# Performance work log

Hardware: AMD Instinct MI355X
Metric: run time of the kernel (lower is better)

## Reference

```python
import jax, jax.numpy as jnp
import numpy as np

B, T, C, H = 4, 4096, 1024, 64

def setup_inputs() -> dict:
    key = jax.random.key(0)
    k1, k2, k3, k4 = jax.random.split(key, 4)
    x = jax.random.normal(k1, (B, T, C), dtype=jnp.float32)
    # Linear(n_embed, head_size, bias=False), stored as [in, out] for x @ W
    s = 1.0 / np.sqrt(C)
    Wq = jax.random.uniform(k2, (C, H), dtype=jnp.float32, minval=-s, maxval=s)
    Wk = jax.random.uniform(k3, (C, H), dtype=jnp.float32, minval=-s, maxval=s)
    Wv = jax.random.uniform(k4, (C, H), dtype=jnp.float32, minval=-s, maxval=s)
    return {"x": x, "Wq": Wq, "Wk": Wk, "Wv": Wv}

def reference(x, Wq, Wk, Wv):
    Bn, Tn, Cn = x.shape
    q = x @ Wq  # [B,T,H]
    k = x @ Wk  # [B,T,H]
    v = x @ Wv  # [B,T,H]
    # NOTE: original scales by C**-0.5 (embedding dim), not head_size**-0.5
    wei = jnp.einsum('bqh,bkh->bqk', q, k) * (Cn ** -0.5)  # [B,T,T]
    causal = jnp.tril(jnp.ones((Tn, Tn), dtype=bool))
    wei = jnp.where(causal, wei, -jnp.inf)
    wei = jax.nn.softmax(wei, axis=-1)
    out = jnp.einsum('bqk,bkh->bqh', wei, v)  # [B,T,H]
    return out
```

## Files before the change

### kernel.cpp

```cpp
#include <hip/hip_runtime.h>
#include <hip/hip_bf16.h>


#define B_DIM 4
#define T_DIM 4096
#define C_DIM 1024
#define H_DIM 64
#define SCALE2 0.0450842066f
#define KP 72

typedef __attribute__((ext_vector_type(8))) short bf8;
typedef __attribute__((ext_vector_type(4))) float f32x4;
typedef __attribute__((ext_vector_type(16))) float f32x16;

__device__ __forceinline__ float fast_exp2(float f) {
    return __builtin_amdgcn_exp2f(f);
}
__device__ __forceinline__ ushort f2bf(float f) {
    union { float f; uint u; } x; x.f = f;
    const uint u = x.u;
    return (ushort)((u + 0x7FFFu + ((u >> 16) & 1u)) >> 16);
}
__device__ __forceinline__ uint cvt_pk_bf16(float lo, float hi) {
    uint r;
    asm("v_cvt_pk_bf16_f32 %0, %1, %2" : "=v"(r) : "v"(lo), "v"(hi));
    return r;
}
__device__ __forceinline__ void permswapf(float& a, float& b) {
    asm volatile("v_permlane32_swap_b32 %0, %1" : "+v"(a), "+v"(b));
}
__device__ __forceinline__ void permswapu(uint& a, uint& b) {
    asm volatile("v_permlane32_swap_b32 %0, %1" : "+v"(a), "+v"(b));
}
__device__ __forceinline__ bf8 frag_from(uint w0, uint w1, uint w2, uint w3) {
    union { uint u[4]; bf8 f; } x;
    x.u[0] = w0; x.u[1] = w1; x.u[2] = w2; x.u[3] = w3;
    return x.f;
}

__global__ __launch_bounds__(256) void wt_kernel(
    const float* __restrict__ Wq, const float* __restrict__ Wk,
    const float* __restrict__ Wv, ushort* __restrict__ wtg)
{
    const int id  = blockIdx.x * 256 + threadIdx.x;
    const int col = id >> 7;
    const int k8  = (id & 127) * 8;
    const int m   = col >> 6, lc = col & 63;
    const float* W = (m == 0) ? Wq : (m == 1) ? Wk : Wv;
    ushort o[8];
    #pragma unroll
    for (int i = 0; i < 8; ++i)
        o[i] = f2bf(W[(size_t)(k8 + i) * H_DIM + lc]);
    *(bf8*)&wtg[(size_t)col * C_DIM + k8] = *(bf8*)o;
}

__global__ __launch_bounds__(256) void qkv_mfma_kernel(
    const float* __restrict__ x, const ushort* __restrict__ wtg,
    ushort* __restrict__ qo, ushort* __restrict__ ko, ushort* __restrict__ vo)
{
    __shared__ ushort xs[32][KP];
    __shared__ ushort wts[192][KP];
    const int t    = threadIdx.x;
    const int lane = t & 63, wave = t >> 6;
    const int g    = lane >> 4, lid = lane & 15;
    const size_t r0 = (size_t)blockIdx.x * 32;

    f32x4 acc[2][3] = {};

    const int xrow = t >> 3, xcol = (t & 7) * 8;
    float4 xr[2];
    bf8 wreg[6];

    xr[0] = *(const float4*)&x[(r0 + xrow) * C_DIM + xcol];
    xr[1] = *(const float4*)&x[(r0 + xrow) * C_DIM + xcol + 4];
    #pragma unroll
    for (int it = 0; it < 6; ++it) {
        const int n = t + it * 256;
        wreg[it] = *(const bf8*)&wtg[(size_t)(n >> 3) * C_DIM + (n & 7) * 8];
    }

    for (int kc = 0; kc < C_DIM / 64; ++kc) {
        __syncthreads();
        {
            uint p[4];
            p[0] = cvt_pk_bf16(xr[0].x, xr[0].y); p[1] = cvt_pk_bf16(xr[0].z, xr[0].w);
            p[2] = cvt_pk_bf16(xr[1].x, xr[1].y); p[3] = cvt_pk_bf16(xr[1].z, xr[1].w);
            *(bf8*)&xs[xrow][xcol] = *(bf8*)p;
            #pragma unroll
            for (int it = 0; it < 6; ++it) {
                const int n = t + it * 256;
                *(bf8*)&wts[n >> 3][(n & 7) * 8] = wreg[it];
            }
        }
        __syncthreads();
        if (kc + 1 < C_DIM / 64) {
            const int kb = (kc + 1) * 64;
            xr[0] = *(const float4*)&x[(r0 + xrow) * C_DIM + kb + xcol];
            xr[1] = *(const float4*)&x[(r0 + xrow) * C_DIM + kb + xcol + 4];
            #pragma unroll
            for (int it = 0; it < 6; ++it) {
                const int n = t + it * 256;
                wreg[it] = *(const bf8*)&wtg[(size_t)(n >> 3) * C_DIM + kb + (n & 7) * 8];
            }
        }
        #pragma unroll
        for (int ks = 0; ks < 2; ++ks) {
            const bf8 a0 = *(const bf8*)&xs[lid][ks * 32 + g * 8];
            const bf8 a1 = *(const bf8*)&xs[16 + lid][ks * 32 + g * 8];
            #pragma unroll
            for (int j = 0; j < 3; ++j) {
                const int ct = wave * 3 + j;
                const bf8 bb = *(const bf8*)&wts[ct * 16 + lid][ks * 32 + g * 8];
                acc[0][j] = __builtin_amdgcn_mfma_f32_16x16x32_bf16(a0, bb, acc[0][j], 0, 0, 0);
                acc[1][j] = __builtin_amdgcn_mfma_f32_16x16x32_bf16(a1, bb, acc[1][j], 0, 0, 0);
            }
        }
    }

    #pragma unroll
    for (int rt = 0; rt < 2; ++rt)
        #pragma unroll
        for (int j = 0; j < 3; ++j) {
            const int ct = wave * 3 + j;
            const int m  = ct >> 2, lc = (ct & 3) * 16 + lid;
            ushort* dst = (m == 0) ? qo : (m == 1) ? ko : vo;
            const float sc = (m == 0) ? SCALE2 : 1.f;
            #pragma unroll
            for (int r = 0; r < 4; ++r) {
                const size_t row = r0 + rt * 16 + 4 * g + r;
                dst[row * H_DIM + lc] = f2bf(acc[rt][j][r] * sc);
            }
        }
}

__global__ __launch_bounds__(256) void flash_mfma_kernel(
    const ushort* __restrict__ q, const ushort* __restrict__ k,
    const ushort* __restrict__ v, float* __restrict__ pO,
    float* __restrict__ pm, float* __restrict__ pl,
    float* __restrict__ out, int S, int nslots, int direct)
{
    const int qt  = 31 - blockIdx.y;
    const int c   = blockIdx.x;
    const int ntk = 2 * qt + 2;
    const int kt_begin = c * S;
    const int kt_end   = min((c + 1) * S, ntk);
    if (kt_begin >= kt_end) return;

    __shared__ ushort ks[64][KP];
    __shared__ ushort vt[64][KP];
    __shared__ float  fsh[4][32];
    __shared__ float  lsh[4][32];

    const int t    = threadIdx.x;
    const int lane = t & 63, wave = t >> 6;
    const int l31  = lane & 31, hi = lane >> 5;
    const int b    = blockIdx.z;
    const int bq0  = qt * 128;
    const int qrow0 = bq0 + wave * 32;
    const int ktw_max = (qrow0 + 31) >> 6;
    const size_t base = (size_t)b * T_DIM * H_DIM;

    bf8 qf[4];
    {
        const size_t qoff = base + (size_t)(qrow0 + l31) * H_DIM + hi * 8;
        #pragma unroll
        for (int kk = 0; kk < 4; ++kk)
            qf[kk] = *(const bf8*)&q[qoff + kk * 16];
    }

    f32x16 oa0 = {}, oa1 = {};
    float m_run = -1e29f, l_run = 0.f;

    const int krow = t >> 2, kc16 = (t & 3) * 16;
    const int vj = (t & 31) * 2, vc = (t >> 5) * 8;
    bf8 kr0, kr1, vr0, vr1;
    {
        const int kg = kt_begin * 64;
        kr0 = *(const bf8*)&k[base + (size_t)(kg + krow) * H_DIM + kc16];
        kr1 = *(const bf8*)&k[base + (size_t)(kg + krow) * H_DIM + kc16 + 8];
        vr0 = *(const bf8*)&v[base + (size_t)(kg + vj) * H_DIM + vc];
        vr1 = *(const bf8*)&v[base + (size_t)(kg + vj + 1) * H_DIM + vc];
    }

    #define BUILD_PA(dst, sv, bofs) do {                                   \
        uint a0_ = cvt_pk_bf16(sv[(bofs)+0], sv[(bofs)+1]);                \
        uint b0_ = cvt_pk_bf16(sv[(bofs)+4], sv[(bofs)+5]);                \
        uint a1_ = cvt_pk_bf16(sv[(bofs)+2], sv[(bofs)+3]);                \
        uint b1_ = cvt_pk_bf16(sv[(bofs)+6], sv[(bofs)+7]);                \
        permswapu(a0_, b0_); permswapu(a1_, b1_);                          \
        dst = frag_from(a0_, a1_, b0_, b1_);                               \
    } while (0)

    for (int kt64 = kt_begin; kt64 < kt_end; ++kt64) {
        __syncthreads();
        *(bf8*)&ks[krow][kc16]     = kr0;
        *(bf8*)&ks[krow][kc16 + 8] = kr1;
        #pragma unroll
        for (int i = 0; i < 8; ++i) {
            const uint pk = (uint)(ushort)vr0[i] | ((uint)(ushort)vr1[i] << 16);
            *(uint*)&vt[vc + i][vj] = pk;
        }
        __syncthreads();
        if (kt64 + 1 < kt_end) {
            const int kg = (kt64 + 1) * 64;
            kr0 = *(const bf8*)&k[base + (size_t)(kg + krow) * H_DIM + kc16];
            kr1 = *(const bf8*)&k[base + (size_t)(kg + krow) * H_DIM + kc16 + 8];
            vr0 = *(const bf8*)&v[base + (size_t)(kg + vj) * H_DIM + vc];
            vr1 = *(const bf8*)&v[base + (size_t)(kg + vj + 1) * H_DIM + vc];
        }
        if (kt64 > ktw_max) continue;

        f32x16 st0 = {}, st1 = {};
        #pragma unroll
        for (int kk = 0; kk < 4; ++kk) {
            const bf8 kfa = *(const bf8*)&ks[l31][kk * 16 + hi * 8];
            st0 = __builtin_amdgcn_mfma_f32_32x32x16_bf16(kfa, qf[kk], st0, 0, 0, 0);
        }
        #pragma unroll
        for (int kk = 0; kk < 4; ++kk) {
            const bf8 kfb = *(const bf8*)&ks[32 + l31][kk * 16 + hi * 8];
            st1 = __builtin_amdgcn_mfma_f32_32x32x16_bf16(kfb, qf[kk], st1, 0, 0, 0);
        }

        if (kt64 * 64 + 63 > qrow0) {
            const int qg  = qrow0 + l31;
            const int kb0 = kt64 * 64 + 4 * hi;
            #pragma unroll
            for (int r = 0; r < 16; ++r) {
                const int key0 = kb0 + (r & 3) + 8 * (r >> 2);
                if (key0 > qg)      st0[r] = -1e30f;
                if (key0 + 32 > qg) st1[r] = -1e30f;
            }
        }

        float mx = st0[0];
        #pragma unroll
        for (int r = 1; r < 16; ++r) mx = fmaxf(mx, st0[r]);
        #pragma unroll
        for (int r = 0; r < 16; ++r) mx = fmaxf(mx, st1[r]);
        { float ma = mx, mb = mx; permswapf(ma, mb); mx = fmaxf(ma, mb); }
        const bool nof = (mx <= m_run + 8.0f);
        const float mnew = nof ? m_run : mx;
        const float fsc  = nof ? 1.0f : fast_exp2(m_run - mnew);
        m_run = mnew;
        float ls = 0.f;
        #pragma unroll
        for (int r = 0; r < 16; ++r) { st0[r] = fast_exp2(st0[r] - mnew); ls += st0[r]; }
        #pragma unroll
        for (int r = 0; r < 16; ++r) { st1[r] = fast_exp2(st1[r] - mnew); ls += st1[r]; }
        { float la = ls, lb = ls; permswapf(la, lb); ls = la + lb; }
        l_run = l_run * fsc + ls;

        bf8 pa[4];
        BUILD_PA(pa[0], st0, 0);
        BUILD_PA(pa[1], st0, 8);
        BUILD_PA(pa[2], st1, 0);
        BUILD_PA(pa[3], st1, 8);

        if (!__all(nof)) {
            if (lane < 32) fsh[wave][l31] = fsc;
            #pragma unroll
            for (int j = 0; j < 4; ++j) {
                const float4 fb = *(const float4*)&fsh[wave][8 * j + 4 * hi];
                oa0[4*j+0] *= fb.x; oa0[4*j+1] *= fb.y; oa0[4*j+2] *= fb.z; oa0[4*j+3] *= fb.w;
                oa1[4*j+0] *= fb.x; oa1[4*j+1] *= fb.y; oa1[4*j+2] *= fb.z; oa1[4*j+3] *= fb.w;
            }
        }

        #pragma unroll
        for (int kk = 0; kk < 4; ++kk) {
            const bf8 vb0 = *(const bf8*)&vt[l31][kk * 16 + hi * 8];
            const bf8 vb1 = *(const bf8*)&vt[32 + l31][kk * 16 + hi * 8];
            oa0 = __builtin_amdgcn_mfma_f32_32x32x16_bf16(pa[kk], vb0, oa0, 0, 0, 0);
            oa1 = __builtin_amdgcn_mfma_f32_32x32x16_bf16(pa[kk], vb1, oa1, 0, 0, 0);
        }
    }
    #undef BUILD_PA

    if (direct) {
        if (lane < 32) lsh[wave][l31] = l_run;
        #pragma unroll
        for (int j = 0; j < 4; ++j) {
            const float4 lv = *(const float4*)&lsh[wave][8 * j + 4 * hi];
            const float iv[4] = {1.f / lv.x, 1.f / lv.y, 1.f / lv.z, 1.f / lv.w};
            #pragma unroll
            for (int rr = 0; rr < 4; ++rr) {
                const size_t rowoff = base + (size_t)(qrow0 + 8 * j + 4 * hi + rr) * H_DIM;
                out[rowoff + l31]      = oa0[4 * j + rr] * iv[rr];
                out[rowoff + 32 + l31] = oa1[4 * j + rr] * iv[rr];
            }
        }
    } else {
        const size_t u = ((size_t)b * 32 + qt) * nslots + c;
        float* po = pO + u * 8192;
        #pragma unroll
        for (int j = 0; j < 4; ++j)
            #pragma unroll
            for (int rr = 0; rr < 4; ++rr) {
                const int row = wave * 32 + 8 * j + 4 * hi + rr;
                po[(size_t)row * 64 + l31]      = oa0[4 * j + rr];
                po[(size_t)row * 64 + 32 + l31] = oa1[4 * j + rr];
            }
        if (lane < 32) {
            pm[u * 128 + wave * 32 + l31] = m_run;
            pl[u * 128 + wave * 32 + l31] = l_run;
        }
    }
}

__global__ __launch_bounds__(256) void combine_kernel(
    const float* __restrict__ pO, const float* __restrict__ pm,
    const float* __restrict__ pl, float* __restrict__ out,
    int S, int nslots)
{
    const int qt = blockIdx.x, b = blockIdx.y;
    const int ntk = 2 * qt + 2;
    const int nch = min(nslots, (ntk + S - 1) / S);
    const int t = threadIdx.x;
    const int row = t >> 1, seg = (t & 1) * 32;
    const size_t u0 = ((size_t)b * 32 + qt) * nslots;

    float M = -1e30f;
    for (int cc = 0; cc < nch; ++cc)
        M = fmaxf(M, pm[(u0 + cc) * 128 + row]);
    float L = 0.f, alpha[8];
    for (int cc = 0; cc < nch; ++cc) {
        alpha[cc] = fast_exp2(pm[(u0 + cc) * 128 + row] - M);
        L += pl[(u0 + cc) * 128 + row] * alpha[cc];
    }
    const float inv = 1.f / L;

    float4 o[8] = {};
    for (int cc = 0; cc < nch; ++cc) {
        const float a = alpha[cc];
        #pragma unroll
        for (int j = 0; j < 8; ++j) {
            const float4 p = *(const float4*)&pO[(u0 + cc) * 8192 +
                                                 (size_t)row * 64 + seg + j * 4];
            o[j].x += p.x * a; o[j].y += p.y * a;
            o[j].z += p.z * a; o[j].w += p.w * a;
        }
    }
    const size_t ob = (size_t)b * T_DIM * H_DIM + (size_t)(qt * 128 + row) * H_DIM + seg;
    #pragma unroll
    for (int j = 0; j < 8; ++j) {
        float4 r;
        r.x = o[j].x * inv; r.y = o[j].y * inv;
        r.z = o[j].z * inv; r.w = o[j].w * inv;
        *(float4*)&out[ob + j * 4] = r;
    }
}

extern "C" void kernel_launch(void* const* d_in, const int* in_sizes, int n_in,
                              void* d_out, int out_size, void* d_ws, size_t ws_size,
                              hipStream_t stream)
{
    const float* x  = (const float*)d_in[0];
    const float* Wq = (const float*)d_in[1];
    const float* Wk = (const float*)d_in[2];
    const float* Wv = (const float*)d_in[3];
    float* out = (float*)d_out;

    const size_t MB = 1u << 20;
    char* ws = (char*)d_ws;
    ushort* qb  = (ushort*)(ws);
    ushort* kb  = (ushort*)(ws + 2 * MB);
    ushort* vb  = (ushort*)(ws + 4 * MB);
    ushort* wtg = (ushort*)(ws + 6 * MB);
    float*  pO  = (float*)(ws + 7 * MB);

    int nslots, S;
    if      (ws_size >= 41 * MB) { nslots = 8; S = 8;  }
    else if (ws_size >= 24 * MB) { nslots = 4; S = 16; }
    else if (ws_size >= 16 * MB) { nslots = 2; S = 32; }
    else                         { nslots = 1; S = 64; }
    const int direct = (nslots == 1);
    float* pm = pO + (size_t)nslots * 1048576;
    float* pl = pm + (size_t)nslots * 16384;

    hipLaunchKernelGGL(wt_kernel, dim3(96), dim3(256), 0, stream, Wq, Wk, Wv, wtg);
    hipLaunchKernelGGL(qkv_mfma_kernel, dim3((B_DIM * T_DIM) / 32), dim3(256),
                       0, stream, x, wtg, qb, kb, vb);
    hipLaunchKernelGGL(flash_mfma_kernel, dim3(nslots, T_DIM / 128, B_DIM), dim3(256),
                       0, stream, qb, kb, vb, pO, pm, pl, out, S, nslots, direct);
    if (!direct)
        hipLaunchKernelGGL(combine_kernel, dim3(T_DIM / 128, B_DIM), dim3(256),
                           0, stream, pO, pm, pl, out, S, nslots);
}
```

Measured before the change: 77.59 us.

## Use single-wave flash blocks loading K and transposed V directly from global

The flash kernel becomes one 64-thread wave per 32-query tile. It no longer stages K/V through shared memory with block-wide barriers; each wave loads K fragments and a pre-transposed V, written transposed by the QKV kernel, straight into registers, with K double-buffered. This removes LDS staging and __syncthreads and gives four times more, finer-grained blocks for causal load balance. The cost is redundant global/L2 reads of K and V per wave, a strided transposed V store in the projection kernel, and a tighter rescale threshold. The combine kernel and partial buffers are resized to match.

Result: slower. 99.53 us (+28.3%).

```diff
diff --git a/kernel.cpp b/kernel.cpp
--- a/kernel.cpp
+++ b/kernel.cpp
@@ -6,6 +6,7 @@
 #define T_DIM 4096
 #define C_DIM 1024
 #define H_DIM 64
+#define NBT   16384
 #define SCALE2 0.0450842066f
 #define KP 72
 
@@ -56,7 +57,7 @@
 
 __global__ __launch_bounds__(256) void qkv_mfma_kernel(
     const float* __restrict__ x, const ushort* __restrict__ wtg,
-    ushort* __restrict__ qo, ushort* __restrict__ ko, ushort* __restrict__ vo)
+    ushort* __restrict__ qo, ushort* __restrict__ ko, ushort* __restrict__ vT)
 {
     __shared__ ushort xs[32][KP];
     __shared__ ushort wts[192][KP];
@@ -123,42 +124,45 @@
         for (int j = 0; j < 3; ++j) {
             const int ct = wave * 3 + j;
             const int m  = ct >> 2, lc = (ct & 3) * 16 + lid;
-            ushort* dst = (m == 0) ? qo : (m == 1) ? ko : vo;
-            const float sc = (m == 0) ? SCALE2 : 1.f;
-            #pragma unroll
-            for (int r = 0; r < 4; ++r) {
-                const size_t row = r0 + rt * 16 + 4 * g + r;
-                dst[row * H_DIM + lc] = f2bf(acc[rt][j][r] * sc);
-            }
-        }
-}
-
-__global__ __launch_bounds__(256) void flash_mfma_kernel(
+            if (m == 2) {
+                ushort4 o;
+                o.x = f2bf(acc[rt][j][0]); o.y = f2bf(acc[rt][j][1]);
+                o.z = f2bf(acc[rt][j][2]); o.w = f2bf(acc[rt][j][3]);
+                *(ushort4*)&vT[(size_t)lc * NBT + r0 + rt * 16 + 4 * g] = o;
+            } else {
+                ushort* dst = (m == 0) ? qo : ko;
+                const float sc = (m == 0) ? SCALE2 : 1.f;
+                #pragma unroll
+                for (int r = 0; r < 4; ++r) {
+                    const size_t row = r0 + rt * 16 + 4 * g + r;
+                    dst[row * H_DIM + lc] = f2bf(acc[rt][j][r] * sc);
+                }
+            }
+        }
+}
+
+__global__ __launch_bounds__(64) void flash_mfma_kernel(
     const ushort* __restrict__ q, const ushort* __restrict__ k,
-    const ushort* __restrict__ v, float* __restrict__ pO,
+    const ushort* __restrict__ vT, float* __restrict__ pO,
     float* __restrict__ pm, float* __restrict__ pl,
     float* __restrict__ out, int S, int nslots, int direct)
 {
-    const int qt  = 31 - blockIdx.y;
+    const int qt  = 127 - blockIdx.y;
     const int c   = blockIdx.x;
-    const int ntk = 2 * qt + 2;
-    const int kt_begin = c * S;
-    const int kt_end   = min((c + 1) * S, ntk);
-    if (kt_begin >= kt_end) return;
-
-    __shared__ ushort ks[64][KP];
-    __shared__ ushort vt[64][KP];
-    __shared__ float  fsh[4][32];
-    __shared__ float  lsh[4][32];
-
-    const int t    = threadIdx.x;
-    const int lane = t & 63, wave = t >> 6;
+    const int ntk = (qt >> 1) + 1;
+    const int kb  = c * S;
+    const int ke  = min((c + 1) * S, ntk);
+    if (kb >= ke) return;
+
+    __shared__ float fsh[32];
+    __shared__ float lsh[32];
+
+    const int lane = threadIdx.x;
     const int l31  = lane & 31, hi = lane >> 5;
     const int b    = blockIdx.z;
-    const int bq0  = qt * 128;
-    const int qrow0 = bq0 + wave * 32;
-    const int ktw_max = (qrow0 + 31) >> 6;
+    const int qrow0 = qt * 32;
     const size_t base = (size_t)b * T_DIM * H_DIM;
+    const ushort* vTb = vT + (size_t)b * T_DIM;
 
     bf8 qf[4];
     {
@@ -171,117 +175,114 @@
     f32x16 oa0 = {}, oa1 = {};
     float m_run = -1e29f, l_run = 0.f;
 
-    const int krow = t >> 2, kc16 = (t & 3) * 16;
-    const int vj = (t & 31) * 2, vc = (t >> 5) * 8;
-    bf8 kr0, kr1, vr0, vr1;
-    {
-        const int kg = kt_begin * 64;
-        kr0 = *(const bf8*)&k[base + (size_t)(kg + krow) * H_DIM + kc16];
-        kr1 = *(const bf8*)&k[base + (size_t)(kg + krow) * H_DIM + kc16 + 8];
-        vr0 = *(const bf8*)&v[base + (size_t)(kg + vj) * H_DIM + vc];
-        vr1 = *(const bf8*)&v[base + (size_t)(kg + vj + 1) * H_DIM + vc];
-    }
-
-    #define BUILD_PA(dst, sv, bofs) do {                                   \
-        uint a0_ = cvt_pk_bf16(sv[(bofs)+0], sv[(bofs)+1]);                \
-        uint b0_ = cvt_pk_bf16(sv[(bofs)+4], sv[(bofs)+5]);                \
-        uint a1_ = cvt_pk_bf16(sv[(bofs)+2], sv[(bofs)+3]);                \
-        uint b1_ = cvt_pk_bf16(sv[(bofs)+6], sv[(bofs)+7]);                \
-        permswapu(a0_, b0_); permswapu(a1_, b1_);                          \
-        dst = frag_from(a0_, a1_, b0_, b1_);                               \
+    bf8 kA0[4], kA1[4], kB0[4], kB1[4];
+    bf8 vb0[4], vb1[4];
+
+    #define LOADK(K0, K1, kt_) do {                                          \
+        const size_t ko_ = base + ((size_t)((kt_) * 64 + l31)) * H_DIM + hi * 8; \
+        _Pragma("unroll")                                                    \
+        for (int kk = 0; kk < 4; ++kk) {                                     \
+            K0[kk] = *(const bf8*)&k[ko_ + kk * 16];                         \
+            K1[kk] = *(const bf8*)&k[ko_ + 32 * H_DIM + kk * 16];            \
+        } } while (0)
+
+    #define LOADV(kt_) do {                                                  \
+        const size_t vo_ = (size_t)l31 * NBT + (kt_) * 64 + hi * 8;          \
+        _Pragma("unroll")                                                    \
+        for (int kk = 0; kk < 4; ++kk) {                                     \
+            vb0[kk] = *(const bf8*)&vTb[vo_ + kk * 16];                      \
+            vb1[kk] = *(const bf8*)&vTb[vo_ + (size_t)32 * NBT + kk * 16];   \
+        } } while (0)
+
+    #define BUILD_PA(dst, sv, bofs) do {                                     \
+        uint a0_ = cvt_pk_bf16(sv[(bofs)+0], sv[(bofs)+1]);                  \
+        uint b0_ = cvt_pk_bf16(sv[(bofs)+4], sv[(bofs)+5]);                  \
+        uint a1_ = cvt_pk_bf16(sv[(bofs)+2], sv[(bofs)+3]);                  \
+        uint b1_ = cvt_pk_bf16(sv[(bofs)+6], sv[(bofs)+7]);                  \
+        permswapu(a0_, b0_); permswapu(a1_, b1_);                            \
+        dst = frag_from(a0_, a1_, b0_, b1_);                                 \
     } while (0)
 
-    for (int kt64 = kt_begin; kt64 < kt_end; ++kt64) {
-        __syncthreads();
-        *(bf8*)&ks[krow][kc16]     = kr0;
-        *(bf8*)&ks[krow][kc16 + 8] = kr1;
-        #pragma unroll
-        for (int i = 0; i < 8; ++i) {
-            const uint pk = (uint)(ushort)vr0[i] | ((uint)(ushort)vr1[i] << 16);
-            *(uint*)&vt[vc + i][vj] = pk;
-        }
-        __syncthreads();
-        if (kt64 + 1 < kt_end) {
-            const int kg = (kt64 + 1) * 64;
-            kr0 = *(const bf8*)&k[base + (size_t)(kg + krow) * H_DIM + kc16];
-            kr1 = *(const bf8*)&k[base + (size_t)(kg + krow) * H_DIM + kc16 + 8];
-            vr0 = *(const bf8*)&v[base + (size_t)(kg + vj) * H_DIM + vc];
-            vr1 = *(const bf8*)&v[base + (size_t)(kg + vj + 1) * H_DIM + vc];
-        }
-        if (kt64 > ktw_max) continue;
-
-        f32x16 st0 = {}, st1 = {};
-        #pragma unroll
-        for (int kk = 0; kk < 4; ++kk) {
-            const bf8 kfa = *(const bf8*)&ks[l31][kk * 16 + hi * 8];
-            st0 = __builtin_amdgcn_mfma_f32_32x32x16_bf16(kfa, qf[kk], st0, 0, 0, 0);
-        }
-        #pragma unroll
-        for (int kk = 0; kk < 4; ++kk) {
-            const bf8 kfb = *(const bf8*)&ks[32 + l31][kk * 16 + hi * 8];
-            st1 = __builtin_amdgcn_mfma_f32_32x32x16_bf16(kfb, qf[kk], st1, 0, 0, 0);
-        }
-
-        if (kt64 * 64 + 63 > qrow0) {
-            const int qg  = qrow0 + l31;
-            const int kb0 = kt64 * 64 + 4 * hi;
-            #pragma unroll
-            for (int r = 0; r < 16; ++r) {
-                const int key0 = kb0 + (r & 3) + 8 * (r >> 2);
-                if (key0 > qg)      st0[r] = -1e30f;
-                if (key0 + 32 > qg) st1[r] = -1e30f;
-            }
-        }
-
-        float mx = st0[0];
-        #pragma unroll
-        for (int r = 1; r < 16; ++r) mx = fmaxf(mx, st0[r]);
-        #pragma unroll
-        for (int r = 0; r < 16; ++r) mx = fmaxf(mx, st1[r]);
-        { float ma = mx, mb = mx; permswapf(ma, mb); mx = fmaxf(ma, mb); }
-        const bool nof = (mx <= m_run + 8.0f);
-        const float mnew = nof ? m_run : mx;
-        const float fsc  = nof ? 1.0f : fast_exp2(m_run - mnew);
-        m_run = mnew;
-        float ls = 0.f;
-        #pragma unroll
-        for (int r = 0; r < 16; ++r) { st0[r] = fast_exp2(st0[r] - mnew); ls += st0[r]; }
-        #pragma unroll
-        for (int r = 0; r < 16; ++r) { st1[r] = fast_exp2(st1[r] - mnew); ls += st1[r]; }
-        { float la = ls, lb = ls; permswapf(la, lb); ls = la + lb; }
-        l_run = l_run * fsc + ls;
-
-        bf8 pa[4];
-        BUILD_PA(pa[0], st0, 0);
-        BUILD_PA(pa[1], st0, 8);
-        BUILD_PA(pa[2], st1, 0);
-        BUILD_PA(pa[3], st1, 8);
-
-        if (!__all(nof)) {
-            if (lane < 32) fsh[wave][l31] = fsc;
-            #pragma unroll
-            for (int j = 0; j < 4; ++j) {
-                const float4 fb = *(const float4*)&fsh[wave][8 * j + 4 * hi];
-                oa0[4*j+0] *= fb.x; oa0[4*j+1] *= fb.y; oa0[4*j+2] *= fb.z; oa0[4*j+3] *= fb.w;
-                oa1[4*j+0] *= fb.x; oa1[4*j+1] *= fb.y; oa1[4*j+2] *= fb.z; oa1[4*j+3] *= fb.w;
-            }
-        }
-
-        #pragma unroll
-        for (int kk = 0; kk < 4; ++kk) {
-            const bf8 vb0 = *(const bf8*)&vt[l31][kk * 16 + hi * 8];
-            const bf8 vb1 = *(const bf8*)&vt[32 + l31][kk * 16 + hi * 8];
-            oa0 = __builtin_amdgcn_mfma_f32_32x32x16_bf16(pa[kk], vb0, oa0, 0, 0, 0);
-            oa1 = __builtin_amdgcn_mfma_f32_32x32x16_bf16(pa[kk], vb1, oa1, 0, 0, 0);
-        }
-    }
+    #define COMPUTE_TILE(K0, K1, kt_) do {                                   \
+        f32x16 st0 = {}, st1 = {};                                           \
+        _Pragma("unroll")                                                    \
+        for (int kk = 0; kk < 4; ++kk)                                       \
+            st0 = __builtin_amdgcn_mfma_f32_32x32x16_bf16(K0[kk], qf[kk], st0, 0, 0, 0); \
+        _Pragma("unroll")                                                    \
+        for (int kk = 0; kk < 4; ++kk)                                       \
+            st1 = __builtin_amdgcn_mfma_f32_32x32x16_bf16(K1[kk], qf[kk], st1, 0, 0, 0); \
+        if ((kt_) == ntk - 1) {         \
+            const int qg  = qrow0 + l31;                                     \
+            const int kb0 = (kt_) * 64 + 4 * hi;                             \
+            _Pragma("unroll")                                                \
+            for (int r = 0; r < 16; ++r) {                                   \
+                const int key0 = kb0 + (r & 3) + 8 * (r >> 2);               \
+                if (key0 > qg)      st0[r] = -1e30f;                         \
+                if (key0 + 32 > qg) st1[r] = -1e30f;                         \
+            }                                                                \
+        }                                                                    \
+        float mx = st0[0];                                                   \
+        _Pragma("unroll")                                                    \
+        for (int r = 1; r < 16; ++r) mx = fmaxf(mx, st0[r]);                 \
+        _Pragma("unroll")                                                    \
+        for (int r = 0; r < 16; ++r) mx = fmaxf(mx, st1[r]);                 \
+        { float ma = mx, mb = mx; permswapf(ma, mb); mx = fmaxf(ma, mb); }   \
+        const bool nof = (mx <= m_run + 4.0f);          \
+        const float mnew = nof ? m_run : mx;                                 \
+        const float fsc  = nof ? 1.0f : fast_exp2(m_run - mnew);             \
+        m_run = mnew;                                                        \
+        float ls = 0.f;                                                      \
+        _Pragma("unroll")                                                    \
+        for (int r = 0; r < 16; ++r) { st0[r] = fast_exp2(st0[r] - mnew); ls += st0[r]; } \
+        _Pragma("unroll")                                                    \
+        for (int r = 0; r < 16; ++r) { st1[r] = fast_exp2(st1[r] - mnew); ls += st1[r]; } \
+        { float la = ls, lb = ls; permswapf(la, lb); ls = la + lb; }         \
+        l_run = l_run * fsc + ls;                                            \
+        bf8 pa[4];                                                           \
+        BUILD_PA(pa[0], st0, 0);                                             \
+        BUILD_PA(pa[1], st0, 8);                                             \
+        BUILD_PA(pa[2], st1, 0);                                             \
+        BUILD_PA(pa[3], st1, 8);                                             \
+        if (!__all(nof)) {                                                   \
+            if (lane < 32) fsh[l31] = fsc;                                   \
+            _Pragma("unroll")                                                \
+            for (int j = 0; j < 4; ++j) {                                    \
+                const float4 fb = *(const float4*)&fsh[8 * j + 4 * hi];      \
+                oa0[4*j+0] *= fb.x; oa0[4*j+1] *= fb.y;                      \
+                oa0[4*j+2] *= fb.z; oa0[4*j+3] *= fb.w;                      \
+                oa1[4*j+0] *= fb.x; oa1[4*j+1] *= fb.y;                      \
+                oa1[4*j+2] *= fb.z; oa1[4*j+3] *= fb.w;                      \
+            }                                                                \
+        }                                                                    \
+        _Pragma("unroll")                                                    \
+        for (int kk = 0; kk < 4; ++kk) {                                     \
+            oa0 = __builtin_amdgcn_mfma_f32_32x32x16_bf16(pa[kk], vb0[kk], oa0, 0, 0, 0); \
+            oa1 = __builtin_amdgcn_mfma_f32_32x32x16_bf16(pa[kk], vb1[kk], oa1, 0, 0, 0); \
+        }                                                                    \
+    } while (0)
+
+    LOADK(kA0, kA1, kb);
+    int kt = kb;
+    for (;;) {
+        LOADV(kt);
+        if (kt + 1 < ke) LOADK(kB0, kB1, kt + 1);
+        COMPUTE_TILE(kA0, kA1, kt);
+        ++kt; if (kt >= ke) break;
+        LOADV(kt);
+        if (kt + 1 < ke) LOADK(kA0, kA1, kt + 1);
+        COMPUTE_TILE(kB0, kB1, kt);
+        ++kt; if (kt >= ke) break;
+    }
+    #undef COMPUTE_TILE
     #undef BUILD_PA
+    #undef LOADV
+    #undef LOADK
 
     if (direct) {
-        if (lane < 32) lsh[wave][l31] = l_run;
+        if (lane < 32) lsh[l31] = l_run;
         #pragma unroll
         for (int j = 0; j < 4; ++j) {
-            const float4 lv = *(const float4*)&lsh[wave][8 * j + 4 * hi];
+            const float4 lv = *(const float4*)&lsh[8 * j + 4 * hi];
             const float iv[4] = {1.f / lv.x, 1.f / lv.y, 1.f / lv.z, 1.f / lv.w};
             #pragma unroll
             for (int rr = 0; rr < 4; ++rr) {
@@ -291,19 +292,19 @@
             }
         }
     } else {
-        const size_t u = ((size_t)b * 32 + qt) * nslots + c;
-        float* po = pO + u * 8192;
+        const size_t u = ((size_t)b * 128 + qt) * nslots + c;
+        float* po = pO + u * 2048;
         #pragma unroll
         for (int j = 0; j < 4; ++j)
             #pragma unroll
             for (int rr = 0; rr < 4; ++rr) {
-                const int row = wave * 32 + 8 * j + 4 * hi + rr;
+                const int row = 8 * j + 4 * hi + rr;
                 po[(size_t)row * 64 + l31]      = oa0[4 * j + rr];
                 po[(size_t)row * 64 + 32 + l31] = oa1[4 * j + rr];
             }
         if (lane < 32) {
-            pm[u * 128 + wave * 32 + l31] = m_run;
-            pl[u * 128 + wave * 32 + l31] = l_run;
+            pm[u * 32 + l31] = m_run;
+            pl[u * 32 + l31] = l_run;
         }
     }
 }
@@ -314,36 +315,36 @@
     int S, int nslots)
 {
     const int qt = blockIdx.x, b = blockIdx.y;
-    const int ntk = 2 * qt + 2;
-    const int nch = min(nslots, (ntk + S - 1) / S);
+    const int ntk = (qt >> 1) + 1;
+    const int nch = (ntk + S - 1) / S;
     const int t = threadIdx.x;
-    const int row = t >> 1, seg = (t & 1) * 32;
-    const size_t u0 = ((size_t)b * 32 + qt) * nslots;
+    const int row = t >> 3, seg = (t & 7) * 8;
+    const size_t u0 = ((size_t)b * 128 + qt) * nslots;
 
     float M = -1e30f;
     for (int cc = 0; cc < nch; ++cc)
-        M = fmaxf(M, pm[(u0 + cc) * 128 + row]);
+        M = fmaxf(M, pm[(u0 + cc) * 32 + row]);
     float L = 0.f, alpha[8];
     for (int cc = 0; cc < nch; ++cc) {
-        alpha[cc] = fast_exp2(pm[(u0 + cc) * 128 + row] - M);
-        L += pl[(u0 + cc) * 128 + row] * alpha[cc];
+        alpha[cc] = fast_exp2(pm[(u0 + cc) * 32 + row] - M);
+        L += pl[(u0 + cc) * 32 + row] * alpha[cc];
     }
     const float inv = 1.f / L;
 
-    float4 o[8] = {};
+    float4 o[2] = {};
     for (int cc = 0; cc < nch; ++cc) {
         const float a = alpha[cc];
         #pragma unroll
-        for (int j = 0; j < 8; ++j) {
-            const float4 p = *(const float4*)&pO[(u0 + cc) * 8192 +
+        for (int j = 0; j < 2; ++j) {
+            const float4 p = *(const float4*)&pO[(u0 + cc) * 2048 +
                                                  (size_t)row * 64 + seg + j * 4];
             o[j].x += p.x * a; o[j].y += p.y * a;
             o[j].z += p.z * a; o[j].w += p.w * a;
         }
     }
-    const size_t ob = (size_t)b * T_DIM * H_DIM + (size_t)(qt * 128 + row) * H_DIM + seg;
+    const size_t ob = (size_t)b * T_DIM * H_DIM + (size_t)(qt * 32 + row) * H_DIM + seg;
     #pragma unroll
-    for (int j = 0; j < 8; ++j) {
+    for (int j = 0; j < 2; ++j) {
         float4 r;
         r.x = o[j].x * inv; r.y = o[j].y * inv;
         r.z = o[j].z * inv; r.w = o[j].w * inv;
@@ -365,7 +366,7 @@
     char* ws = (char*)d_ws;
     ushort* qb  = (ushort*)(ws);
     ushort* kb  = (ushort*)(ws + 2 * MB);
-    ushort* vb  = (ushort*)(ws + 4 * MB);
+    ushort* vTb = (ushort*)(ws + 4 * MB);
     ushort* wtg = (ushort*)(ws + 6 * MB);
     float*  pO  = (float*)(ws + 7 * MB);
 
@@ -380,10 +381,10 @@
 
     hipLaunchKernelGGL(wt_kernel, dim3(96), dim3(256), 0, stream, Wq, Wk, Wv, wtg);
     hipLaunchKernelGGL(qkv_mfma_kernel, dim3((B_DIM * T_DIM) / 32), dim3(256),
-                       0, stream, x, wtg, qb, kb, vb);
-    hipLaunchKernelGGL(flash_mfma_kernel, dim3(nslots, T_DIM / 128, B_DIM), dim3(256),
-                       0, stream, qb, kb, vb, pO, pm, pl, out, S, nslots, direct);
+                       0, stream, x, wtg, qb, kb, vTb);
+    hipLaunchKernelGGL(flash_mfma_kernel, dim3(nslots, T_DIM / 32, B_DIM), dim3(64),
+                       0, stream, qb, kb, vTb, pO, pm, pl, out, S, nslots, direct);
     if (!direct)
-        hipLaunchKernelGGL(combine_kernel, dim3(T_DIM / 128, B_DIM), dim3(256),
+        hipLaunchKernelGGL(combine_kernel, dim3(T_DIM / 32, B_DIM), dim3(256),
                            0, stream, pO, pm, pl, out, S, nslots);
 }
```
